# Kernel tuning notes

Hardware: AMD Instinct MI355X
Metric: run time of the kernel (lower is better)

## Reference

```python
import jax, jax.numpy as jnp
import numpy as np

B, N, D, DH = 2, 256, 256, 256


def setup_inputs() -> dict:
    key = jax.random.key(0)
    ks = jax.random.split(key, 8)
    s = 1.0 / np.sqrt(D)
    return {
        "x": jax.random.normal(ks[0], (B, N, D), dtype=jnp.float32),
        "e": jax.random.normal(ks[1], (B, N, N, D), dtype=jnp.float32),
        "Wq": jax.random.normal(ks[2], (D, DH), dtype=jnp.float32) * s,
        "bq": jnp.zeros((DH,), dtype=jnp.float32),
        "Wk": jax.random.normal(ks[3], (D, DH), dtype=jnp.float32) * s,
        "bk": jnp.zeros((DH,), dtype=jnp.float32),
        "Wv": jax.random.normal(ks[4], (D, DH), dtype=jnp.float32) * s,
        "bv": jnp.zeros((DH,), dtype=jnp.float32),
    }


def reference(x, e, Wq, bq, Wk, bk, Wv, bv):
    # Q_edge: [B, N, N, DH]; indexed Q[b, j, i, :]
    Q = jnp.einsum("bjid,dh->bjih", e, Wq) + bq
    K = x @ Wk + bk  # [B, N, DH]
    V = x @ Wv + bv  # [B, N, DH]
    scale = 1.0 / jnp.sqrt(jnp.asarray(Q.shape[-1], Q.dtype))
    # K_i[b,j,i] = K[b,i];  K_j[b,j,i] = K[b,j]  (torch expand semantics)
    att_i = jnp.exp(jnp.einsum("bjih,bih->bji", Q, K) * scale)
    att_j = jnp.exp(jnp.einsum("bjih,bjh->bji", Q, K) * scale)
    att_sum = att_i + att_j
    ai = att_i / att_sum  # dropout with p=0.0 is identity
    aj = att_j / att_sum
    # e_out[b,j,i] = ai*V[b,i] + aj*V[b,j]
    e_out = ai[..., None] * V[:, None, :, :] + aj[..., None] * V[:, :, None, :]
    return (x, e_out)
```

## Files before the change

### kernel.cpp

```cpp
#include <hip/hip_runtime.h>
#include <hip/hip_bf16.h>

typedef float nt4 __attribute__((ext_vector_type(4)));

constexpr int Bc  = 2;
constexpr int Nc  = 256;
constexpr int Dc  = 256;
constexpr int DHc = 256;

__global__ __launch_bounds__(256)
void prep_gvc(const float* __restrict__ x,
              const float* __restrict__ Wq, const float* __restrict__ bq,
              const float* __restrict__ Wk, const float* __restrict__ bk,
              const float* __restrict__ Wv, const float* __restrict__ bv,
              float* __restrict__ G, float* __restrict__ V, float* __restrict__ cc,
              float* __restrict__ xout) {
    constexpr int RPB = 4;
    constexpr float scale = 0.0625f;
    __shared__ float xs[RPB][Dc];
    __shared__ float ks[RPB][DHc];
    const int r0 = blockIdx.x * RPB;
    const int dd = threadIdx.x;

    #pragma unroll
    for (int rr = 0; rr < RPB; ++rr) {
        float xv = x[(size_t)(r0 + rr) * Dc + dd];
        xs[rr][dd] = xv;
        xout[(size_t)(r0 + rr) * Dc + dd] = xv;
    }
    __syncthreads();

    float ka[RPB], va[RPB];
    {
        float bkv = bk[dd], bvv = bv[dd];
        #pragma unroll
        for (int rr = 0; rr < RPB; ++rr) { ka[rr] = bkv; va[rr] = bvv; }
    }
    #pragma unroll 4
    for (int d0 = 0; d0 < Dc; ++d0) {
        float wk = Wk[(size_t)d0 * DHc + dd];
        float wv = Wv[(size_t)d0 * DHc + dd];
        #pragma unroll
        for (int rr = 0; rr < RPB; ++rr) {
            ka[rr] += xs[rr][d0] * wk;
            va[rr] += xs[rr][d0] * wv;
        }
    }
    #pragma unroll
    for (int rr = 0; rr < RPB; ++rr) {
        ks[rr][dd] = ka[rr];
        V[(size_t)(r0 + rr) * DHc + dd] = va[rr];
    }
    __syncthreads();

    float ga[RPB] = {};
    #pragma unroll 8
    for (int h = 0; h < DHc; ++h) {
        float wq = Wq[(size_t)dd * DHc + h];
        #pragma unroll
        for (int rr = 0; rr < RPB; ++rr) ga[rr] += ks[rr][h] * wq;
    }
    #pragma unroll
    for (int rr = 0; rr < RPB; ++rr)
        G[(size_t)(r0 + rr) * Dc + dd] = ga[rr] * scale;

    {
        int rr = dd >> 6, l = dd & 63;
        float p = 0.f;
        #pragma unroll
        for (int k = 0; k < 4; ++k) p += ks[rr][l + 64 * k] * bq[l + 64 * k];
        #pragma unroll
        for (int m = 1; m < 64; m <<= 1) p += __shfl_xor(p, m, 64);
        if (l == 0) cc[r0 + rr] = p * scale;
    }
}

__global__ __launch_bounds__(256, 4)
void edge_main(const float* __restrict__ e,
               const float* __restrict__ G,
               const float* __restrict__ V,
               const float* __restrict__ cc,
               float* __restrict__ eout) {
    const int W = blockIdx.x * 4 + (threadIdx.x >> 6);
    const int l = threadIdx.x & 63;
    const int b   = W >> 11;
    const int rem = W & 2047;
    const int j   = rem >> 3;
    const int s   = rem & 7;
    const int i0  = s * 32;

    const size_t nb = (size_t)b * Nc;
    const float4* G4 = reinterpret_cast<const float4*>(G);
    const float4* V4 = reinterpret_cast<const float4*>(V);

    const float4 gj = G4[(nb + j) * 64 + l];
    const float4 vj = V4[(nb + j) * 64 + l];
    const float  cj = cc[nb + j];

    const float4* e4 = reinterpret_cast<const float4*>(e) +
                       (((size_t)b * Nc + j) * Nc + i0) * 64 + l;
    float4* o4 = reinterpret_cast<float4*>(eout) +
                 (((size_t)b * Nc + j) * Nc + i0) * 64 + l;
    const float4* Gi = G4 + (nb + i0) * 64 + l;
    const float4* Vi = V4 + (nb + i0) * 64 + l;
    const float*  ccp = cc + nb + i0;

    float4 ev = e4[0], gi = Gi[0], vi = Vi[0];
    float  ci = ccp[0];

    #pragma unroll
    for (int t = 0; t < 32; ++t) {
        float4 nev, ngi, nvi;
        float  nci;
        if (t < 31) {
            nev = e4[(size_t)(t + 1) * 64];
            ngi = Gi[(size_t)(t + 1) * 64];
            nvi = Vi[(size_t)(t + 1) * 64];
            nci = ccp[t + 1];
        }
        float si = ev.x * gi.x + ev.y * gi.y + ev.z * gi.z + ev.w * gi.w;
        float sj = ev.x * gj.x + ev.y * gj.y + ev.z * gj.z + ev.w * gj.w;
        #pragma unroll
        for (int m = 1; m < 64; m <<= 1) {
            si += __shfl_xor(si, m, 64);
            sj += __shfl_xor(sj, m, 64);
        }
        si += ci;
        sj += cj;
        const float ai = 1.f / (1.f + __expf(sj - si));
        const float aj = 1.f - ai;

        nt4 o;
        o.x = ai * vi.x + aj * vj.x;
        o.y = ai * vi.y + aj * vj.y;
        o.z = ai * vi.z + aj * vj.z;
        o.w = ai * vi.w + aj * vj.w;
        __builtin_nontemporal_store(o, reinterpret_cast<nt4*>(&o4[(size_t)t * 64]));

        ev = nev; gi = ngi; vi = nvi; ci = nci;
    }
}

extern "C" void kernel_launch(void* const* d_in, const int* in_sizes, int n_in,
                              void* d_out, int out_size, void* d_ws, size_t ws_size,
                              hipStream_t stream) {
    const float* x  = (const float*)d_in[0];
    const float* e  = (const float*)d_in[1];
    const float* Wq = (const float*)d_in[2];
    const float* bq = (const float*)d_in[3];
    const float* Wk = (const float*)d_in[4];
    const float* bk = (const float*)d_in[5];
    const float* Wv = (const float*)d_in[6];
    const float* bv = (const float*)d_in[7];
    float* out = (float*)d_out;

    float* G  = (float*)d_ws;
    float* V  = G + (size_t)Bc * Nc * Dc;
    float* cc = V + (size_t)Bc * Nc * DHc;

    prep_gvc<<<Bc * Nc / 4, 256, 0, stream>>>(x, Wq, bq, Wk, bk, Wv, bv,
                                              G, V, cc, out);
    edge_main<<<Bc * Nc * 8 / 4, 256, 0, stream>>>(
        e, G, V, cc, out + (size_t)Bc * Nc * Dc);
}
```

Before: 295.8 us.

## Split edge kernel into score and combine passes with DPP 16-lane reductions

Splits the fused edge kernel into two kernels. The first computes the attention weights, with each 16-lane group handling one edge row and reducing through DPP row operations in place of a full 64-lane shuffle reduction. The second reads the stored weights back with readlane and writes the blended V outputs. This cuts the cross-lane reduction cost and separates the e-read stream from the output-write stream. In exchange it adds a kernel launch, an intermediate weight buffer round-trip, and drops the explicit software prefetch.

```diff
diff --git a/kernel.cpp b/kernel.cpp
--- a/kernel.cpp
+++ b/kernel.cpp
@@ -7,6 +7,15 @@
 constexpr int Nc  = 256;
 constexpr int Dc  = 256;
 constexpr int DHc = 256;
+
+__device__ __forceinline__ float dpp_sum16(float v) {
+    float t;
+    t = __int_as_float(__builtin_amdgcn_mov_dpp(__float_as_int(v), 0xB1, 0xF, 0xF, true)); v += t;
+    t = __int_as_float(__builtin_amdgcn_mov_dpp(__float_as_int(v), 0x4E, 0xF, 0xF, true)); v += t;
+    t = __int_as_float(__builtin_amdgcn_mov_dpp(__float_as_int(v), 0x141, 0xF, 0xF, true)); v += t;
+    t = __int_as_float(__builtin_amdgcn_mov_dpp(__float_as_int(v), 0x140, 0xF, 0xF, true)); v += t;
+    return v;
+}
 
 __global__ __launch_bounds__(256)
 void prep_gvc(const float* __restrict__ x,
@@ -75,69 +84,99 @@
     }
 }
 
-__global__ __launch_bounds__(256, 4)
-void edge_main(const float* __restrict__ e,
-               const float* __restrict__ G,
-               const float* __restrict__ V,
-               const float* __restrict__ cc,
-               float* __restrict__ eout) {
+__global__ __launch_bounds__(256)
+void score_pass(const float* __restrict__ e,
+                const float* __restrict__ G,
+                const float* __restrict__ cc,
+                float* __restrict__ ai_out) {
     const int W = blockIdx.x * 4 + (threadIdx.x >> 6);
     const int l = threadIdx.x & 63;
-    const int b   = W >> 11;
-    const int rem = W & 2047;
-    const int j   = rem >> 3;
-    const int s   = rem & 7;
-    const int i0  = s * 32;
+    const int b   = W >> 12;
+    const int rem = W & 4095;
+    const int j   = rem >> 4;
+    const int seg = rem & 15;
+    const int g   = l >> 4;
+    const int c4  = l & 15;
+    const int r0  = seg * 16;
 
     const size_t nb = (size_t)b * Nc;
     const float4* G4 = reinterpret_cast<const float4*>(G);
+
+    const float4 gj0 = G4[(nb + j) * 64 + c4];
+    const float4 gj1 = G4[(nb + j) * 64 + c4 + 16];
+    const float4 gj2 = G4[(nb + j) * 64 + c4 + 32];
+    const float4 gj3 = G4[(nb + j) * 64 + c4 + 48];
+    const float  cj  = cc[nb + j];
+
+    const float4* e4  = reinterpret_cast<const float4*>(e) +
+                        (((size_t)b * Nc + j) * Nc + r0) * 64;
+    const float4* Gi  = G4 + (nb + r0) * 64;
+    const float*  ccp = cc + nb + r0;
+    float* aout = ai_out + ((size_t)b * Nc + j) * Nc + r0;
+
+    #pragma unroll
+    for (int t = 0; t < 4; ++t) {
+        const int r = t * 4 + g;
+        const float ci = ccp[r];
+        float4 ev0 = e4[(size_t)r * 64 + c4];
+        float4 ev1 = e4[(size_t)r * 64 + c4 + 16];
+        float4 ev2 = e4[(size_t)r * 64 + c4 + 32];
+        float4 ev3 = e4[(size_t)r * 64 + c4 + 48];
+        float4 gi0 = Gi[(size_t)r * 64 + c4];
+        float4 gi1 = Gi[(size_t)r * 64 + c4 + 16];
+        float4 gi2 = Gi[(size_t)r * 64 + c4 + 32];
+        float4 gi3 = Gi[(size_t)r * 64 + c4 + 48];
+
+        float si, sj;
+        si  = ev0.x * gi0.x + ev0.y * gi0.y + ev0.z * gi0.z + ev0.w * gi0.w;
+        si += ev1.x * gi1.x + ev1.y * gi1.y + ev1.z * gi1.z + ev1.w * gi1.w;
+        si += ev2.x * gi2.x + ev2.y * gi2.y + ev2.z * gi2.z + ev2.w * gi2.w;
+        si += ev3.x * gi3.x + ev3.y * gi3.y + ev3.z * gi3.z + ev3.w * gi3.w;
+        sj  = ev0.x * gj0.x + ev0.y * gj0.y + ev0.z * gj0.z + ev0.w * gj0.w;
+        sj += ev1.x * gj1.x + ev1.y * gj1.y + ev1.z * gj1.z + ev1.w * gj1.w;
+        sj += ev2.x * gj2.x + ev2.y * gj2.y + ev2.z * gj2.z + ev2.w * gj2.w;
+        sj += ev3.x * gj3.x + ev3.y * gj3.y + ev3.z * gj3.z + ev3.w * gj3.w;
+
+        si = dpp_sum16(si) + ci;
+        sj = dpp_sum16(sj) + cj;
+        const float ai = 1.f / (1.f + __expf(sj - si));
+        if (c4 == 0) aout[r] = ai;
+    }
+}
+
+__global__ __launch_bounds__(256)
+void combine_pass(const float* __restrict__ ai_in,
+                  const float* __restrict__ V,
+                  float* __restrict__ eout) {
+    const int W = blockIdx.x * 4 + (threadIdx.x >> 6);
+    const int l = threadIdx.x & 63;
+    const int b   = W >> 12;
+    const int rem = W & 4095;
+    const int j   = rem >> 4;
+    const int seg = rem & 15;
+    const int r0  = seg * 16;
+
+    const size_t nb = (size_t)b * Nc;
     const float4* V4 = reinterpret_cast<const float4*>(V);
-
-    const float4 gj = G4[(nb + j) * 64 + l];
     const float4 vj = V4[(nb + j) * 64 + l];
-    const float  cj = cc[nb + j];
-
-    const float4* e4 = reinterpret_cast<const float4*>(e) +
-                       (((size_t)b * Nc + j) * Nc + i0) * 64 + l;
+    const float  av = ai_in[((size_t)b * Nc + j) * Nc + r0 + (l & 15)];
+
+    const float4* Vi = V4 + (nb + r0) * 64 + l;
     float4* o4 = reinterpret_cast<float4*>(eout) +
-                 (((size_t)b * Nc + j) * Nc + i0) * 64 + l;
-    const float4* Gi = G4 + (nb + i0) * 64 + l;
-    const float4* Vi = V4 + (nb + i0) * 64 + l;
-    const float*  ccp = cc + nb + i0;
-
-    float4 ev = e4[0], gi = Gi[0], vi = Vi[0];
-    float  ci = ccp[0];
-
-    #pragma unroll
-    for (int t = 0; t < 32; ++t) {
-        float4 nev, ngi, nvi;
-        float  nci;
-        if (t < 31) {
-            nev = e4[(size_t)(t + 1) * 64];
-            ngi = Gi[(size_t)(t + 1) * 64];
-            nvi = Vi[(size_t)(t + 1) * 64];
-            nci = ccp[t + 1];
-        }
-        float si = ev.x * gi.x + ev.y * gi.y + ev.z * gi.z + ev.w * gi.w;
-        float sj = ev.x * gj.x + ev.y * gj.y + ev.z * gj.z + ev.w * gj.w;
-        #pragma unroll
-        for (int m = 1; m < 64; m <<= 1) {
-            si += __shfl_xor(si, m, 64);
-            sj += __shfl_xor(sj, m, 64);
-        }
-        si += ci;
-        sj += cj;
-        const float ai = 1.f / (1.f + __expf(sj - si));
+                 (((size_t)b * Nc + j) * Nc + r0) * 64 + l;
+
+    #pragma unroll
+    for (int t = 0; t < 16; ++t) {
+        const float ai = __int_as_float(
+            __builtin_amdgcn_readlane(__float_as_int(av), t));
         const float aj = 1.f - ai;
-
+        const float4 vi = Vi[(size_t)t * 64];
         nt4 o;
         o.x = ai * vi.x + aj * vj.x;
         o.y = ai * vi.y + aj * vj.y;
         o.z = ai * vi.z + aj * vj.z;
         o.w = ai * vi.w + aj * vj.w;
         __builtin_nontemporal_store(o, reinterpret_cast<nt4*>(&o4[(size_t)t * 64]));
-
-        ev = nev; gi = ngi; vi = nvi; ci = nci;
     }
 }
 
@@ -157,9 +196,12 @@
     float* G  = (float*)d_ws;
     float* V  = G + (size_t)Bc * Nc * Dc;
     float* cc = V + (size_t)Bc * Nc * DHc;
+    float* ai = cc + (size_t)Bc * Nc;
+
+    float* eo = out + (size_t)Bc * Nc * Dc;
 
     prep_gvc<<<Bc * Nc / 4, 256, 0, stream>>>(x, Wq, bq, Wk, bk, Wv, bv,
                                               G, V, cc, out);
-    edge_main<<<Bc * Nc * 8 / 4, 256, 0, stream>>>(
-        e, G, V, cc, out + (size_t)Bc * Nc * Dc);
-}
+    score_pass<<<Bc * Nc * 16 / 4, 256, 0, stream>>>(e, G, cc, ai);
+    combine_pass<<<Bc * Nc * 16 / 4, 256, 0, stream>>>(ai, V, eo);
+}
```

New measurement: 291.0 us. About the same (-1.6%).
